# Kernel optimization log

Hardware: AMD Instinct MI355X
Metric: run time of the kernel (lower is better)

The kernel has to match this reference:

```python
import jax, jax.numpy as jnp
import numpy as np

DECAY = 0.99


def setup_inputs() -> dict:
    key = jax.random.key(0)
    k1, k2, k3 = jax.random.split(key, 3)
    B, D, H, W = 16, 128, 32, 32
    K = 8192
    z_e = jax.random.normal(k1, (B, D, H, W), dtype=jnp.float32)
    codebook = jax.random.normal(k2, (K, D), dtype=jnp.float32)
    ema_count = jnp.ones((K,), dtype=jnp.float32)
    ema_weight = codebook  # buffer initialized as codebook.clone()
    return {"z_e": z_e, "codebook": codebook, "ema_count": ema_count, "ema_weight": ema_weight}


def reference(z_e, codebook, ema_count, ema_weight):
    B, D, H, W = z_e.shape
    K = codebook.shape[0]
    # (B,D,H,W) -> (N,D)
    z_flat = z_e.transpose(0, 2, 3, 1).reshape(-1, D)
    # squared L2 distances: ||z||^2 - 2 z.C^T + ||C||^2  -> (N,K)
    dist = (
        jnp.sum(z_flat * z_flat, axis=1, keepdims=True)
        - 2.0 * (z_flat @ codebook.T)
        + jnp.sum(codebook * codebook, axis=1)[None, :]
    )
    indices = jnp.argmin(dist, axis=1)  # (N,)
    z_q = codebook[indices].reshape(B, H, W, D).transpose(0, 3, 1, 2)
    # EMA codebook update (training path, no grad)
    counts = jax.ops.segment_sum(jnp.ones_like(indices, dtype=jnp.float32), indices, num_segments=K)
    dw = jax.ops.segment_sum(z_flat, indices, num_segments=K)  # (K,D)
    new_count = ema_count * DECAY + (1.0 - DECAY) * counts
    new_weight = ema_weight * DECAY + (1.0 - DECAY) * dw
    new_codebook = new_weight / jnp.maximum(new_count, 1.0)[:, None]
    # straight-through estimator
    z_q_st = z_e + jax.lax.stop_gradient(z_q - z_e)
    return (z_q_st, indices.reshape(B, H, W), new_codebook, new_count, new_weight)
```

## Files before the change

### kernel.cpp

```cpp
#include <hip/hip_runtime.h>

#define D 128
#define HW 1024
#define NROWS 16384
#define K 8192
#define NU 32

#define OUT0 0
#define OUT1 2097152
#define OUT2 2113536
#define OUT3 3162112
#define OUT4 3170304

typedef __attribute__((ext_vector_type(8))) _Float16 half8;
typedef __attribute__((ext_vector_type(16))) float f32x16;
typedef unsigned short u16;
typedef unsigned long long u64;

__device__ __forceinline__ void gld16(const u16* gsrc, u16* ldst) {
    __builtin_amdgcn_global_load_lds(
        (const __attribute__((address_space(1))) unsigned int*)gsrc,
        (__attribute__((address_space(3))) unsigned int*)ldst,
        16, 0, 0);
}

__global__ __launch_bounds__(256) void k_prep_cb(const float* __restrict__ cb,
                                                 u16* __restrict__ Bg,
                                                 float* __restrict__ cnorm,
                                                 u64* __restrict__ packed,
                                                 float* __restrict__ counts,
                                                 float* __restrict__ dw) {
    const int tid = threadIdx.x;
    int kk = tid & 15;
    int k = blockIdx.x * 16 + (tid >> 4);
    const float* src = cb + (size_t)k * D + kk * 8;
    half8 h, l;
    float s = 0.f;
#pragma unroll
    for (int j = 0; j < 8; ++j) {
        float v = src[j];
        s += v * v;
        _Float16 hv = (_Float16)v;
        _Float16 lv = (_Float16)(v - (float)hv);
        h[j] = hv;
        l[j] = lv;
    }
    int g = k >> 6, col = k & 63;
    size_t offH = (size_t)g * 16384 + ((size_t)kk * 64 + col) * 8;
    *(half8*)((_Float16*)Bg + offH) = h;
    *(half8*)((_Float16*)Bg + offH + 8192) = l;
#pragma unroll
    for (int off = 8; off > 0; off >>= 1) s += __shfl_down(s, off);
    if (kk == 0) cnorm[k] = s;
    float4 z4 = {0.f, 0.f, 0.f, 0.f};
    size_t zi = ((size_t)blockIdx.x * 256 + tid) * 8;
    *(float4*)(dw + zi) = z4;
    *(float4*)(dw + zi + 4) = z4;
    if (blockIdx.x < 64) packed[blockIdx.x * 256 + tid] = ~0ull;
    else if (blockIdx.x < 96) counts[(blockIdx.x - 64) * 256 + tid] = 0.f;
}

__global__ __launch_bounds__(256, 2) void k_argmin_mfma(
        const float* __restrict__ z_e,
        const u16* __restrict__ Bg,
        const float* __restrict__ cnorm, u64* __restrict__ packed) {
    __shared__ u16 lds[2][16384];

    const int tid = threadIdx.x;
    const int ln  = tid & 63;
    const int l31 = ln & 31;
    const int lh  = ln >> 5;
    const int wy  = (tid >> 6) & 1;
    const int wx  = tid >> 7;

    const int rg = blockIdx.x >> 2;
    const int k0 = (blockIdx.x & 3) * 2048;
    const int g0 = k0 >> 6;

    half8 Ah[2][8], Al[2][8];
#pragma unroll
    for (int rt = 0; rt < 2; ++rt) {
        const int rowA = rg * 128 + wy * 64 + rt * 32 + l31;
        const float* za = z_e + (size_t)(rowA >> 10) * (D * HW) + (rowA & 1023);
#pragma unroll
        for (int ks = 0; ks < 8; ++ks) {
            half8 h, l;
#pragma unroll
            for (int j = 0; j < 8; ++j) {
                float v = za[(size_t)(ks * 16 + lh * 8 + j) * HW];
                _Float16 hv = (_Float16)v;
                _Float16 lv = (_Float16)(v - (float)hv);
                h[j] = hv;
                l[j] = lv;
            }
            Ah[rt][ks] = h;
            Al[rt][ks] = l;
        }
    }

    {
        const u16* src = Bg + (size_t)g0 * 16384;
#pragma unroll
        for (int r = 0; r < 8; ++r)
            gld16(src + (r * 256 + tid) * 8, lds[0] + (r * 256 + tid) * 8);
    }

    float minv[2][16];
    int   mini[2][16];
#pragma unroll
    for (int rt = 0; rt < 2; ++rt)
#pragma unroll
        for (int r = 0; r < 16; ++r) { minv[rt][r] = INFINITY; mini[rt][r] = 0; }

    const int bo_base = wx * 32 + l31;

#pragma unroll 1
    for (int u = 0; u < NU; ++u) {
        const int colv = k0 + u * 64 + wx * 32 + l31;
        float cn0 = cnorm[colv];

        if (u + 1 < NU) {
            const u16* src = Bg + (size_t)(g0 + u + 1) * 16384;
            u16* dst = lds[(u + 1) & 1];
#pragma unroll
            for (int r = 0; r < 8; ++r)
                gld16(src + (r * 256 + tid) * 8, dst + (r * 256 + tid) * 8);
            asm volatile("s_waitcnt vmcnt(8)" ::: "memory");
        } else {
            asm volatile("s_waitcnt vmcnt(0)" ::: "memory");
        }
        asm volatile("s_barrier" ::: "memory");

        const _Float16* bh = (const _Float16*)lds[u & 1];
        const _Float16* bl = bh + 8192;
        f32x16 acc0 = {}, acc1 = {};
#pragma unroll
        for (int ks = 0; ks < 8; ++ks) {
            const int bo = ((ks * 2 + lh) * 64 + bo_base) * 8;
            half8 vbl = *(const half8*)(bl + bo);
            half8 vbh = *(const half8*)(bh + bo);
            acc0 = __builtin_amdgcn_mfma_f32_32x32x16_f16(Ah[0][ks], vbl, acc0, 0, 0, 0);
            acc1 = __builtin_amdgcn_mfma_f32_32x32x16_f16(Ah[1][ks], vbl, acc1, 0, 0, 0);
            acc0 = __builtin_amdgcn_mfma_f32_32x32x16_f16(Ah[0][ks], vbh, acc0, 0, 0, 0);
            acc1 = __builtin_amdgcn_mfma_f32_32x32x16_f16(Ah[1][ks], vbh, acc1, 0, 0, 0);
            acc0 = __builtin_amdgcn_mfma_f32_32x32x16_f16(Al[0][ks], vbh, acc0, 0, 0, 0);
            acc1 = __builtin_amdgcn_mfma_f32_32x32x16_f16(Al[1][ks], vbh, acc1, 0, 0, 0);
        }

#pragma unroll
        for (int r = 0; r < 16; ++r) {
            float d0 = fmaf(-2.0f, acc0[r], cn0);
            float d1 = fmaf(-2.0f, acc1[r], cn0);
            if (d0 < minv[0][r]) { minv[0][r] = d0; mini[0][r] = colv; }
            if (d1 < minv[1][r]) { minv[1][r] = d1; mini[1][r] = colv; }
        }
        asm volatile("s_barrier" ::: "memory");
    }

#pragma unroll
    for (int rt = 0; rt < 2; ++rt)
#pragma unroll
        for (int r = 0; r < 16; ++r) {
            float v = minv[rt][r];
            int ix = mini[rt][r];
#pragma unroll
            for (int off = 1; off < 32; off <<= 1) {
                float v2 = __shfl_xor(v, off);
                int i2 = __shfl_xor(ix, off);
                if (v2 < v || (v2 == v && i2 < ix)) { v = v2; ix = i2; }
            }
            if (l31 == 0) {
                int row = rg * 128 + wy * 64 + rt * 32 + 4 * lh + (r & 3) + 8 * (r >> 2);
                unsigned int uenc = __float_as_uint(v);
                uenc = (uenc & 0x80000000u) ? ~uenc : (uenc | 0x80000000u);
                u64 pk = ((u64)uenc << 13) | (u64)(unsigned)ix;
                atomicMin(&packed[row], pk);
            }
        }
}

__global__ __launch_bounds__(256) void k_epilogue(const float* __restrict__ z_e,
                                                  const float* __restrict__ cb,
                                                  const u64* __restrict__ packed,
                                                  float* __restrict__ out0,
                                                  float* __restrict__ out1,
                                                  float* __restrict__ counts,
                                                  float* __restrict__ dw) {
    __shared__ int idxS[64];
    const int tid = threadIdx.x;
    const int n0 = blockIdx.x * 64;
    const int bb = n0 >> 10, p0 = n0 & 1023;

    if (tid < 64) {
        int ix = (int)(packed[n0 + tid] & 0x1FFFull);
        idxS[tid] = ix;
        out1[n0 + tid] = (float)ix;
        atomicAdd(&counts[ix], 1.0f);
    }
    __syncthreads();

    const float* zb = z_e + (size_t)bb * (D * HW) + p0;
    float* ob = out0 + (size_t)bb * (D * HW) + p0;

    for (int i = tid; i < 64 * D; i += 256) {
        int d = i >> 6, r = i & 63;
        float z = zb[(size_t)d * HW + r];
        float c = cb[(size_t)idxS[r] * D + d];
        ob[(size_t)d * HW + r] = z + (c - z);
    }
    for (int i = tid; i < 64 * D; i += 256) {
        int r = i >> 7, d = i & 127;
        atomicAdd(&dw[(size_t)idxS[r] * D + d], zb[(size_t)d * HW + r]);
    }
}

__global__ __launch_bounds__(256) void k_final(const float* __restrict__ ema_count,
                                               const float* __restrict__ ema_weight,
                                               float* __restrict__ out2,
                                               float* __restrict__ out3,
                                               float* __restrict__ out4) {
    int gid = blockIdx.x * 256 + threadIdx.x;
    int k = gid >> 7, d = gid & 127;
    float cnt_raw = out3[k];
    float dw_raw = out4[gid];
    __syncthreads();
    float nc = 0.99f * ema_count[k] + 0.01f * cnt_raw;
    float nw = 0.99f * ema_weight[gid] + 0.01f * dw_raw;
    out4[gid] = nw;
    out2[gid] = nw / fmaxf(nc, 1.0f);
    if (d == 0) out3[k] = nc;
}

extern "C" void kernel_launch(void* const* d_in, const int* in_sizes, int n_in,
                              void* d_out, int out_size, void* d_ws, size_t ws_size,
                              hipStream_t stream) {
    const float* z_e        = (const float*)d_in[0];
    const float* cb         = (const float*)d_in[1];
    const float* ema_count  = (const float*)d_in[2];
    const float* ema_weight = (const float*)d_in[3];
    float* out = (float*)d_out;

    float* cnorm = (float*)d_ws;
    u64* packed = (u64*)((char*)d_ws + K * 4);

    u16* Bg = (u16*)(out + OUT2);

    k_prep_cb    <<<K / 16,        256, 0, stream>>>(cb, Bg, cnorm, packed,
                                                     out + OUT3, out + OUT4);
    k_argmin_mfma<<<512,           256, 0, stream>>>(z_e, Bg, cnorm, packed);
    k_epilogue   <<<NROWS / 64,    256, 0, stream>>>(z_e, cb, packed,
                                                     out + OUT0, out + OUT1,
                                                     out + OUT3, out + OUT4);
    k_final      <<<(K * D) / 256, 256, 0, stream>>>(ema_count, ema_weight,
                                                     out + OUT2, out + OUT3, out + OUT4);
}
```

Baseline: 209.7 us.

## Sort rows by code index for segmented dw reduction, widen argmin blocks

Replaces per-element float atomics into dw with a counting sort: count per code, scan offsets, scatter row ids, then each wave sums runs of rows sharing a code before issuing one atomic per run. The z rows are transposed once into a row-major scratch buffer placed in out0, which is overwritten later by the straight-through output. The argmin kernel moves to 512-thread blocks, each covering 256 rows and 1024 codes, so every codebook tile in LDS serves twice as many rows. The cost is three extra small launches, including a single-block scan, plus the transpose pass.

```diff
diff --git a/kernel.cpp b/kernel.cpp
--- a/kernel.cpp
+++ b/kernel.cpp
@@ -4,7 +4,7 @@
 #define HW 1024
 #define NROWS 16384
 #define K 8192
-#define NU 32
+#define NU 16
 
 #define OUT0 0
 #define OUT1 2097152
@@ -12,9 +12,18 @@
 #define OUT3 3162112
 #define OUT4 3170304
 
+#define WS_CNORM   0
+#define WS_PACKED  32768
+#define WS_CNT     163840
+#define WS_CNT2    196608
+#define WS_OFFS    229376
+#define WS_IDX16   262400
+#define WS_ROWLIST 295424
+
 typedef __attribute__((ext_vector_type(8))) _Float16 half8;
 typedef __attribute__((ext_vector_type(16))) float f32x16;
 typedef unsigned short u16;
+typedef unsigned int u32;
 typedef unsigned long long u64;
 
 __device__ __forceinline__ void gld16(const u16* gsrc, u16* ldst) {
@@ -28,7 +37,8 @@
                                                  u16* __restrict__ Bg,
                                                  float* __restrict__ cnorm,
                                                  u64* __restrict__ packed,
-                                                 float* __restrict__ counts,
+                                                 u32* __restrict__ cnt,
+                                                 u32* __restrict__ cnt2,
                                                  float* __restrict__ dw) {
     const int tid = threadIdx.x;
     int kk = tid & 15;
@@ -56,11 +66,12 @@
     size_t zi = ((size_t)blockIdx.x * 256 + tid) * 8;
     *(float4*)(dw + zi) = z4;
     *(float4*)(dw + zi + 4) = z4;
-    if (blockIdx.x < 64) packed[blockIdx.x * 256 + tid] = ~0ull;
-    else if (blockIdx.x < 96) counts[(blockIdx.x - 64) * 256 + tid] = 0.f;
-}
-
-__global__ __launch_bounds__(256, 2) void k_argmin_mfma(
+    int gid = blockIdx.x * 256 + tid;
+    if (gid < NROWS) packed[gid] = ~0ull;
+    if (gid < K) { cnt[gid] = 0u; cnt2[gid] = 0u; }
+}
+
+__global__ __launch_bounds__(512, 4) void k_argmin_mfma(
         const float* __restrict__ z_e,
         const u16* __restrict__ Bg,
         const float* __restrict__ cnorm, u64* __restrict__ packed) {
@@ -70,17 +81,18 @@
     const int ln  = tid & 63;
     const int l31 = ln & 31;
     const int lh  = ln >> 5;
-    const int wy  = (tid >> 6) & 1;
-    const int wx  = tid >> 7;
-
-    const int rg = blockIdx.x >> 2;
-    const int k0 = (blockIdx.x & 3) * 2048;
+    const int wv  = tid >> 6;
+    const int wy  = wv & 3;
+    const int wx  = wv >> 2;
+
+    const int rg = blockIdx.x >> 3;
+    const int k0 = (blockIdx.x & 7) * 1024;
     const int g0 = k0 >> 6;
 
     half8 Ah[2][8], Al[2][8];
 #pragma unroll
     for (int rt = 0; rt < 2; ++rt) {
-        const int rowA = rg * 128 + wy * 64 + rt * 32 + l31;
+        const int rowA = rg * 256 + wy * 64 + rt * 32 + l31;
         const float* za = z_e + (size_t)(rowA >> 10) * (D * HW) + (rowA & 1023);
 #pragma unroll
         for (int ks = 0; ks < 8; ++ks) {
@@ -101,8 +113,8 @@
     {
         const u16* src = Bg + (size_t)g0 * 16384;
 #pragma unroll
-        for (int r = 0; r < 8; ++r)
-            gld16(src + (r * 256 + tid) * 8, lds[0] + (r * 256 + tid) * 8);
+        for (int r = 0; r < 4; ++r)
+            gld16(src + (r * 512 + tid) * 8, lds[0] + (r * 512 + tid) * 8);
     }
 
     float minv[2][16];
@@ -123,9 +135,9 @@
             const u16* src = Bg + (size_t)(g0 + u + 1) * 16384;
             u16* dst = lds[(u + 1) & 1];
 #pragma unroll
-            for (int r = 0; r < 8; ++r)
-                gld16(src + (r * 256 + tid) * 8, dst + (r * 256 + tid) * 8);
-            asm volatile("s_waitcnt vmcnt(8)" ::: "memory");
+            for (int r = 0; r < 4; ++r)
+                gld16(src + (r * 512 + tid) * 8, dst + (r * 512 + tid) * 8);
+            asm volatile("s_waitcnt vmcnt(4)" ::: "memory");
         } else {
             asm volatile("s_waitcnt vmcnt(0)" ::: "memory");
         }
@@ -170,7 +182,7 @@
                 if (v2 < v || (v2 == v && i2 < ix)) { v = v2; ix = i2; }
             }
             if (l31 == 0) {
-                int row = rg * 128 + wy * 64 + rt * 32 + 4 * lh + (r & 3) + 8 * (r >> 2);
+                int row = rg * 256 + wy * 64 + rt * 32 + 4 * lh + (r & 3) + 8 * (r >> 2);
                 unsigned int uenc = __float_as_uint(v);
                 uenc = (uenc & 0x80000000u) ? ~uenc : (uenc | 0x80000000u);
                 u64 pk = ((u64)uenc << 13) | (u64)(unsigned)ix;
@@ -179,56 +191,140 @@
         }
 }
 
-__global__ __launch_bounds__(256) void k_epilogue(const float* __restrict__ z_e,
-                                                  const float* __restrict__ cb,
-                                                  const u64* __restrict__ packed,
-                                                  float* __restrict__ out0,
-                                                  float* __restrict__ out1,
-                                                  float* __restrict__ counts,
-                                                  float* __restrict__ dw) {
-    __shared__ int idxS[64];
+__global__ __launch_bounds__(256) void k_phase1(const float* __restrict__ z_e,
+                                                const u64* __restrict__ packed,
+                                                float* __restrict__ out1,
+                                                u32* __restrict__ cnt,
+                                                u16* __restrict__ idx16,
+                                                float* __restrict__ zf) {
+    __shared__ float Zt[64 * 132];
     const int tid = threadIdx.x;
     const int n0 = blockIdx.x * 64;
     const int bb = n0 >> 10, p0 = n0 & 1023;
 
     if (tid < 64) {
         int ix = (int)(packed[n0 + tid] & 0x1FFFull);
-        idxS[tid] = ix;
+        idx16[n0 + tid] = (u16)ix;
         out1[n0 + tid] = (float)ix;
-        atomicAdd(&counts[ix], 1.0f);
+        atomicAdd(&cnt[ix], 1u);
+    }
+
+    const float* zb = z_e + (size_t)bb * (D * HW) + p0;
+    for (int i = tid; i < 2048; i += 256) {
+        int d = i >> 4;
+        int r4 = (i & 15) << 2;
+        float4 v = *(const float4*)(zb + (size_t)d * HW + r4);
+        Zt[(r4 + 0) * 132 + d] = v.x;
+        Zt[(r4 + 1) * 132 + d] = v.y;
+        Zt[(r4 + 2) * 132 + d] = v.z;
+        Zt[(r4 + 3) * 132 + d] = v.w;
     }
     __syncthreads();
-
-    const float* zb = z_e + (size_t)bb * (D * HW) + p0;
-    float* ob = out0 + (size_t)bb * (D * HW) + p0;
-
-    for (int i = tid; i < 64 * D; i += 256) {
-        int d = i >> 6, r = i & 63;
-        float z = zb[(size_t)d * HW + r];
-        float c = cb[(size_t)idxS[r] * D + d];
-        ob[(size_t)d * HW + r] = z + (c - z);
-    }
-    for (int i = tid; i < 64 * D; i += 256) {
-        int r = i >> 7, d = i & 127;
-        atomicAdd(&dw[(size_t)idxS[r] * D + d], zb[(size_t)d * HW + r]);
-    }
-}
-
-__global__ __launch_bounds__(256) void k_final(const float* __restrict__ ema_count,
-                                               const float* __restrict__ ema_weight,
-                                               float* __restrict__ out2,
-                                               float* __restrict__ out3,
-                                               float* __restrict__ out4) {
-    int gid = blockIdx.x * 256 + threadIdx.x;
-    int k = gid >> 7, d = gid & 127;
-    float cnt_raw = out3[k];
-    float dw_raw = out4[gid];
+    for (int i = tid; i < 2048; i += 256) {
+        int r = i >> 5, dq = (i & 31) << 2;
+        float4 v = *(const float4*)(&Zt[r * 132 + dq]);
+        *(float4*)(zf + (size_t)(n0 + r) * D + dq) = v;
+    }
+}
+
+__global__ __launch_bounds__(256) void k_scan(const u32* __restrict__ cnt,
+                                              u32* __restrict__ offs) {
+    __shared__ u32 ssum[256];
+    const int t = threadIdx.x;
+    u32 s = 0;
+    for (int j = 0; j < 32; ++j) s += cnt[t * 32 + j];
+    ssum[t] = s;
     __syncthreads();
-    float nc = 0.99f * ema_count[k] + 0.01f * cnt_raw;
-    float nw = 0.99f * ema_weight[gid] + 0.01f * dw_raw;
-    out4[gid] = nw;
-    out2[gid] = nw / fmaxf(nc, 1.0f);
-    if (d == 0) out3[k] = nc;
+    u32 acc = s;
+    for (int off = 1; off < 256; off <<= 1) {
+        u32 v = (t >= off) ? ssum[t - off] : 0u;
+        __syncthreads();
+        acc += v;
+        ssum[t] = acc;
+        __syncthreads();
+    }
+    u32 run = acc - s;
+    for (int j = 0; j < 32; ++j) {
+        offs[t * 32 + j] = run;
+        run += cnt[t * 32 + j];
+    }
+    if (t == 255) offs[K] = run;
+}
+
+__global__ __launch_bounds__(256) void k_scatter(const u16* __restrict__ idx16,
+                                                 const u32* __restrict__ offs,
+                                                 u32* __restrict__ cnt2,
+                                                 u16* __restrict__ rowlist) {
+    int n = blockIdx.x * 256 + threadIdx.x;
+    int ix = idx16[n];
+    u32 pos = offs[ix] + atomicAdd(&cnt2[ix], 1u);
+    rowlist[pos] = (u16)n;
+}
+
+__global__ __launch_bounds__(256) void k_dw(const float* __restrict__ zf,
+                                            const u16* __restrict__ rowlist,
+                                            const u16* __restrict__ idx16,
+                                            float* __restrict__ dw) {
+    const int tid = threadIdx.x;
+    const int ln = tid & 63;
+    const int w = (blockIdx.x * 256 + tid) >> 6;
+    float a0 = 0.f, a1 = 0.f;
+    int prev = -1;
+    for (int i = w * 16; i < w * 16 + 16; ++i) {
+        int n = rowlist[i];
+        int k = idx16[n];
+        float v0 = zf[(size_t)n * D + ln];
+        float v1 = zf[(size_t)n * D + ln + 64];
+        if (k != prev) {
+            if (prev >= 0) {
+                atomicAdd(&dw[(size_t)prev * D + ln], a0);
+                atomicAdd(&dw[(size_t)prev * D + ln + 64], a1);
+            }
+            prev = k; a0 = v0; a1 = v1;
+        } else {
+            a0 += v0; a1 += v1;
+        }
+    }
+    if (prev >= 0) {
+        atomicAdd(&dw[(size_t)prev * D + ln], a0);
+        atomicAdd(&dw[(size_t)prev * D + ln + 64], a1);
+    }
+}
+
+__global__ __launch_bounds__(256) void k_last(const float* __restrict__ z_e,
+                                              const float* __restrict__ cb,
+                                              const u16* __restrict__ idx16,
+                                              const u32* __restrict__ cnt,
+                                              const float* __restrict__ ema_count,
+                                              const float* __restrict__ ema_weight,
+                                              float* __restrict__ out0,
+                                              float* __restrict__ out2,
+                                              float* __restrict__ out3,
+                                              float* __restrict__ out4) {
+    const int tid = threadIdx.x;
+    if (blockIdx.x < 256) {
+        __shared__ int idxS[64];
+        const int n0 = blockIdx.x * 64;
+        const int bb = n0 >> 10, p0 = n0 & 1023;
+        if (tid < 64) idxS[tid] = idx16[n0 + tid];
+        __syncthreads();
+        const float* zb = z_e + (size_t)bb * (D * HW) + p0;
+        float* ob = out0 + (size_t)bb * (D * HW) + p0;
+        for (int i = tid; i < 64 * D; i += 256) {
+            int d = i >> 6, r = i & 63;
+            float z = zb[(size_t)d * HW + r];
+            float c = cb[(size_t)idxS[r] * D + d];
+            ob[(size_t)d * HW + r] = z + (c - z);
+        }
+    } else {
+        int gid = (blockIdx.x - 256) * 256 + tid;
+        int k = gid >> 7, d = gid & 127;
+        float nc = 0.99f * ema_count[k] + 0.01f * (float)cnt[k];
+        float nw = 0.99f * ema_weight[gid] + 0.01f * out4[gid];
+        out4[gid] = nw;
+        out2[gid] = nw / fmaxf(nc, 1.0f);
+        if (d == 0) out3[k] = nc;
+    }
 }
 
 extern "C" void kernel_launch(void* const* d_in, const int* in_sizes, int n_in,
@@ -239,18 +335,29 @@
     const float* ema_count  = (const float*)d_in[2];
     const float* ema_weight = (const float*)d_in[3];
     float* out = (float*)d_out;
-
-    float* cnorm = (float*)d_ws;
-    u64* packed = (u64*)((char*)d_ws + K * 4);
+    char* ws = (char*)d_ws;
+
+    float* cnorm   = (float*)(ws + WS_CNORM);
+    u64*   packed  = (u64*)(ws + WS_PACKED);
+    u32*   cnt     = (u32*)(ws + WS_CNT);
+    u32*   cnt2    = (u32*)(ws + WS_CNT2);
+    u32*   offs    = (u32*)(ws + WS_OFFS);
+    u16*   idx16   = (u16*)(ws + WS_IDX16);
+    u16*   rowlist = (u16*)(ws + WS_ROWLIST);
 
     u16* Bg = (u16*)(out + OUT2);
-
-    k_prep_cb    <<<K / 16,        256, 0, stream>>>(cb, Bg, cnorm, packed,
-                                                     out + OUT3, out + OUT4);
-    k_argmin_mfma<<<512,           256, 0, stream>>>(z_e, Bg, cnorm, packed);
-    k_epilogue   <<<NROWS / 64,    256, 0, stream>>>(z_e, cb, packed,
-                                                     out + OUT0, out + OUT1,
-                                                     out + OUT3, out + OUT4);
-    k_final      <<<(K * D) / 256, 256, 0, stream>>>(ema_count, ema_weight,
-                                                     out + OUT2, out + OUT3, out + OUT4);
-}
+    float* zf = out + OUT0;
+
+    k_prep_cb    <<<K / 16,     256, 0, stream>>>(cb, Bg, cnorm, packed, cnt, cnt2,
+                                                  out + OUT4);
+    k_argmin_mfma<<<512,        512, 0, stream>>>(z_e, Bg, cnorm, packed);
+    k_phase1     <<<NROWS / 64, 256, 0, stream>>>(z_e, packed, out + OUT1, cnt,
+                                                  idx16, zf);
+    k_scan       <<<1,          256, 0, stream>>>(cnt, offs);
+    k_scatter    <<<NROWS / 256,256, 0, stream>>>(idx16, offs, cnt2, rowlist);
+    k_dw         <<<256,        256, 0, stream>>>(zf, rowlist, idx16, out + OUT4);
+    k_last       <<<256 + (K * D) / 256, 256, 0, stream>>>(z_e, cb, idx16, cnt,
+                                                  ema_count, ema_weight,
+                                                  out + OUT0, out + OUT2,
+                                                  out + OUT3, out + OUT4);
+}
```

Result: slower. 481.1 us (+129.4%).
